# Performance work log

Measured on AMD Instinct MI355X. Metric: run time of the kernel, lower is better.

The kernel has to match this reference:

```python
import jax, jax.numpy as jnp
import numpy as np

B, S, D = 2, 2048, 2048
H, KVH, HD = 16, 4, 128
M = 2  # modalities
THETA = 10000.0
REP = H // KVH


def make_freq_cis(seq_len, head_dim, theta):
    # (S, head_dim//2, 2, 2) rotation matrices [[cos,-sin],[sin,cos]]
    inv = theta ** (-jnp.arange(0, head_dim, 2, dtype=jnp.float32) / head_dim)
    ang = jnp.arange(seq_len, dtype=jnp.float32)[:, None] * inv[None, :]  # (S, hd/2)
    c, s = jnp.cos(ang), jnp.sin(ang)
    row0 = jnp.stack([c, -s], axis=-1)
    row1 = jnp.stack([s, c], axis=-1)
    return jnp.stack([row0, row1], axis=-2)  # (S, hd/2, 2, 2)


def setup_inputs() -> dict:
    key = jax.random.key(0)
    ks = jax.random.split(key, 7)
    std = D ** -0.5
    x = jax.random.normal(ks[0], (B, S, D), dtype=jnp.float32)
    freq_cis = make_freq_cis(S, HD, THETA)
    modality_ids = jax.random.randint(ks[1], (B, S), 0, M, dtype=jnp.int32)
    wq = jax.random.normal(ks[2], (M, D, H * HD), dtype=jnp.float32) * std
    wk = jax.random.normal(ks[3], (M, D, KVH * HD), dtype=jnp.float32) * std
    wv = jax.random.normal(ks[4], (M, D, KVH * HD), dtype=jnp.float32) * std
    wo = jax.random.normal(ks[5], (M, H * HD, D), dtype=jnp.float32) * std
    return {"x": x, "freq_cis": freq_cis, "modality_ids": modality_ids,
            "wq": wq, "wk": wk, "wv": wv, "wo": wo}


def apply_rope(t, freq_cis):
    # t: (B, S, h, HD); freq_cis: (S, HD//2, 2, 2)
    b, s, h, hd = t.shape
    t2 = t.reshape(b, s, h, hd // 2, 2)
    out = jnp.einsum('bshdk,sdjk->bshdj', t2, freq_cis)
    return out.reshape(b, s, h, hd)


def reference(x, freq_cis, modality_ids, wq, wk, wv, wo):
    bsz, seq, dim = x.shape
    onehot = jax.nn.one_hot(modality_ids, M, dtype=x.dtype)  # (B,S,M)
    # per-modality QKV projection, then combine (masks partition tokens)
    q = jnp.einsum('bsm,bsd,mdo->bso', onehot, x, wq).reshape(bsz, seq, H, HD)
    k = jnp.einsum('bsm,bsd,mdo->bso', onehot, x, wk).reshape(bsz, seq, KVH, HD)
    v = jnp.einsum('bsm,bsd,mdo->bso', onehot, x, wv).reshape(bsz, seq, KVH, HD)
    q = apply_rope(q, freq_cis)
    k = apply_rope(k, freq_cis)
    # GQA: repeat_interleave kv heads along head dim
    k = jnp.repeat(k, REP, axis=2)
    v = jnp.repeat(v, REP, axis=2)
    scale = 1.0 / jnp.sqrt(jnp.asarray(HD, dtype=x.dtype))
    scores = jnp.einsum('bqhd,bkhd->bhqk', q, k) * scale
    causal = jnp.tril(jnp.ones((seq, seq), dtype=bool))
    scores = jnp.where(causal[None, None], scores, jnp.finfo(x.dtype).min)
    probs = jax.nn.softmax(scores, axis=-1)
    attn = jnp.einsum('bhqk,bkhd->bqhd', probs, v).reshape(bsz, seq, H * HD)
    # per-modality output projection
    out = jnp.einsum('bsm,bso,moe->bse', onehot, attn, wo)
    return out
```

## Files before the change

### kernel.cpp

```cpp
#include <hip/hip_runtime.h>
#include <stdint.h>

typedef unsigned short u16;
typedef __bf16  bf16x8 __attribute__((ext_vector_type(8), may_alias));
typedef u16     u16x8  __attribute__((ext_vector_type(8), may_alias));
typedef float   f32x4  __attribute__((ext_vector_type(4)));
typedef float   f32x4u __attribute__((ext_vector_type(4), may_alias));

#define Bv   2
#define Sv   2048
#define Dv   2048
#define Hv   16
#define KVHv 4
#define HDv  128
#define Tv   (Bv*Sv)
#define QKVN 3072
#define MAXROWS 4352

__device__ __forceinline__ float b2f(u16 u) {
    union { float f; uint32_t i; } x; x.i = ((uint32_t)u) << 16; return x.f;
}
__device__ __forceinline__ u16 f2b(float f) {
    union { float f; uint32_t u; } x; x.f = f;
    uint32_t r = x.u + 0x7fff + ((x.u >> 16) & 1);
    return (u16)(r >> 16);
}
__device__ __forceinline__ void gload_lds16(const void* g, void* l) {
    __builtin_amdgcn_global_load_lds((__attribute__((address_space(1))) void*)(uintptr_t)g,
                                     (__attribute__((address_space(3))) void*)(uintptr_t)l,
                                     16, 0, 0);
}

__global__ __launch_bounds__(1024) void scan_mod(const int* __restrict__ mod, int* __restrict__ fwd,
                                                 int* __restrict__ inv, int* __restrict__ hdr) {
    __shared__ int cnt[1024];
    const int tid = threadIdx.x;
    int m[4]; int c = 0;
#pragma unroll
    for (int e = 0; e < 4; ++e) { m[e] = mod[tid * 4 + e]; c += (m[e] == 0); }
    cnt[tid] = c;
    __syncthreads();
    for (int off = 1; off < 1024; off <<= 1) {
        int v = (tid >= off) ? cnt[tid - off] : 0;
        __syncthreads();
        cnt[tid] += v;
        __syncthreads();
    }
    const int c0 = cnt[1023];
    const int c0pad = (c0 + 255) & ~255;
    const int c1 = Tv - c0;
    const int total = c0pad + ((c1 + 255) & ~255);
    for (int p = tid; p < MAXROWS; p += 1024) inv[p] = -1;
    __syncthreads();
    const int ex0 = cnt[tid] - c;
    int z = 0;
#pragma unroll
    for (int e = 0; e < 4; ++e) {
        int t = tid * 4 + e;
        int pos;
        if (m[e] == 0) { pos = ex0 + z; ++z; }
        else           { pos = c0pad + (t - (ex0 + z)); }
        fwd[t] = pos;
        inv[pos] = t;
    }
    if (tid == 0) { hdr[0] = total >> 8; hdr[1] = c0pad; hdr[2] = total; }
}

__global__ void gather_cast(const float* __restrict__ x, const int* __restrict__ inv,
                            u16* __restrict__ Xg) {
    int v = blockIdx.x * 256 + threadIdx.x;
    int pos = v >> 8, c8 = (v & 255) * 8;
    int t = inv[pos];
    u16x8 val = {0, 0, 0, 0, 0, 0, 0, 0};
    if (t >= 0) {
        f32x4u a = *(const f32x4u*)&x[(size_t)t * Dv + c8];
        f32x4u b = *(const f32x4u*)&x[(size_t)t * Dv + c8 + 4];
#pragma unroll
        for (int j = 0; j < 4; ++j) { val[j] = f2b(a[j]); val[4 + j] = f2b(b[j]); }
    }
    *(u16x8*)&Xg[(size_t)pos * Dv + c8] = val;
}

__global__ void transpose_cast(const float* __restrict__ in, u16* __restrict__ out, int C,
                               size_t inZ, size_t outZ) {
    in  += (size_t)blockIdx.z * inZ;
    out += (size_t)blockIdx.z * outZ;
    __shared__ u16 tile[64][72];
    const int tr = blockIdx.y * 64, tc = blockIdx.x * 64;
    const int tid = threadIdx.x;
#pragma unroll
    for (int i = 0; i < 4; ++i) {
        int s = tid + 256 * i;
        int r = s >> 4, c4 = (s & 15) * 4;
        f32x4u v = *(const f32x4u*)&in[(size_t)(tr + r) * C + tc + c4];
#pragma unroll
        for (int j = 0; j < 4; ++j) tile[r][c4 + j] = f2b(v[j]);
    }
    __syncthreads();
#pragma unroll
    for (int i = 0; i < 2; ++i) {
        int s = tid + 256 * i;
        int r = s >> 3, c8 = (s & 7) * 8;
        u16x8 v;
#pragma unroll
        for (int j = 0; j < 8; ++j) v[j] = tile[c8 + j][r];
        *(u16x8*)&out[(size_t)(tc + r) * 2048 + tr + c8] = v;
    }
}

__device__ __forceinline__ void store_c(u16* C, size_t idx, float v) { C[idx] = f2b(v); }
__device__ __forceinline__ void store_c(float* C, size_t idx, float v) { C[idx] = v; }

template <typename OutT>
__global__ __launch_bounds__(512, 2) void gemm256(const u16* __restrict__ A,
                                                  const u16* __restrict__ Bt,
                                                  OutT* __restrict__ C,
                                                  const int* __restrict__ inv,
                                                  const int* __restrict__ hdr,
                                                  int Nfull, int ldC) {
    const int total = hdr[2], c0pad = hdr[1];
    const int bm = blockIdx.y * 256;
    if (bm >= total) return;
    const u16* B = Bt + (size_t)((bm >= c0pad) ? 1 : 0) * Nfull * 2048;
    const int bn = blockIdx.x * 256;
    const int tid = threadIdx.x;
    const int wave = tid >> 6, lane = tid & 63;
    const int l15 = lane & 15, l4 = lane >> 4;
    const int wm = wave >> 2;
    const int wn = wave & 3;
    const int bhh = wn >> 1, brr = (wn & 1) * 64;
    const int rsw = l15 & 7;
    __shared__ u16 ldsA[2][2][128 * 64];
    __shared__ u16 ldsB[2][2][128 * 64];
    const int srow = tid >> 3;
    const int ssw  = (tid & 7) ^ (srow & 7);
    const int wofs = wave * 8 * 64;

    f32x4 acc[8][4] = {};

    auto stA = [&](int sl, int h, int jrb, int kt) {
        gload_lds16(A + (size_t)(bm + h * 128 + jrb * 64 + srow) * 2048 + kt * 64 + ssw * 8,
                    &ldsA[sl][h][jrb * 64 * 64 + wofs]);
    };
    auto stB = [&](int sl, int h, int jrb, int kt) {
        gload_lds16(B + (size_t)(bn + h * 128 + jrb * 64 + srow) * 2048 + kt * 64 + ssw * 8,
                    &ldsB[sl][h][jrb * 64 * 64 + wofs]);
    };

    stB(0, 0, 0, 0); stB(0, 0, 1, 0); stB(0, 1, 0, 0); stB(0, 1, 1, 0);
    stA(0, 0, 0, 0); stA(0, 1, 0, 0); stA(0, 0, 1, 0); stA(0, 1, 1, 0);
    asm volatile("s_waitcnt vmcnt(2)" ::: "memory");
    __builtin_amdgcn_s_barrier();
    __builtin_amdgcn_sched_barrier(0);

    for (int kt = 0; kt < 32; ++kt) {
        const int s = kt & 1;
        const bool st = (kt < 31);
        bf16x8 bfr[4][2];
#pragma unroll
        for (int fj = 0; fj < 4; ++fj)
#pragma unroll
            for (int kc = 0; kc < 2; ++kc)
                bfr[fj][kc] = *(const bf16x8*)&ldsB[s][bhh][(brr + fj * 16 + l15) * 64 + ((kc * 4 + l4) ^ rsw) * 8];
#pragma unroll
        for (int q = 0; q < 4; ++q) {
            bf16x8 af[2][2];
#pragma unroll
            for (int fi = 0; fi < 2; ++fi)
#pragma unroll
                for (int kc = 0; kc < 2; ++kc)
                    af[fi][kc] = *(const bf16x8*)&ldsA[s][wm][(q * 32 + fi * 16 + l15) * 64 + ((kc * 4 + l4) ^ rsw) * 8];
            if (st) {
                if      (q == 0) { stB(s ^ 1, 0, 0, kt + 1); stB(s ^ 1, 0, 1, kt + 1); }
                else if (q == 1) { stB(s ^ 1, 1, 0, kt + 1); stB(s ^ 1, 1, 1, kt + 1); }
                else if (q == 2) { stA(s ^ 1, 0, 0, kt + 1); stA(s ^ 1, 1, 0, kt + 1); }
                else             { stA(s ^ 1, 0, 1, kt + 1); stA(s ^ 1, 1, 1, kt + 1); }
            }
            __builtin_amdgcn_s_setprio(1);
#pragma unroll
            for (int kc = 0; kc < 2; ++kc)
#pragma unroll
                for (int fi = 0; fi < 2; ++fi)
#pragma unroll
                    for (int fj = 0; fj < 4; ++fj)
                        acc[q * 2 + fi][fj] = __builtin_amdgcn_mfma_f32_16x16x32_bf16(
                            af[fi][kc], bfr[fj][kc], acc[q * 2 + fi][fj], 0, 0, 0);
            __builtin_amdgcn_s_setprio(0);
            if (q == 1) {
                if (st) asm volatile("s_waitcnt vmcnt(4)" ::: "memory");
                else    asm volatile("s_waitcnt vmcnt(0)" ::: "memory");
                __builtin_amdgcn_sched_barrier(0);
            }
            if (q == 3 && st) {
                asm volatile("s_waitcnt vmcnt(2)" ::: "memory");
                __builtin_amdgcn_sched_barrier(0);
            }
            __builtin_amdgcn_s_barrier();
            __builtin_amdgcn_sched_barrier(0);
        }
    }
#pragma unroll
    for (int fi = 0; fi < 8; ++fi)
#pragma unroll
        for (int r = 0; r < 4; ++r) {
            int row = bm + wm * 128 + fi * 16 + l4 * 4 + r;
            int t = inv[row];
            if (t >= 0) {
#pragma unroll
                for (int fj = 0; fj < 4; ++fj) {
                    int col = bn + wn * 64 + fj * 16 + l15;
                    store_c(C, (size_t)t * ldC + col, acc[fi][fj][r]);
                }
            }
        }
}

__global__ void rope_kernel(u16* __restrict__ QKV, const float* __restrict__ fc) {
    int p = blockIdx.x * 256 + threadIdx.x;
    const int t = p / 1280;
    const int r = p - t * 1280;
    const int s = t & (Sv - 1);
    int col, d2; float scale;
    if (r < 1024) { col = 2 * r;                d2 = r & 63;  scale = 0.12751742f; }
    else          { int rr = r - 1024; col = 2048 + 2 * rr; d2 = rr & 63; scale = 1.0f; }
    u16* ptr = QKV + (size_t)t * QKVN + col;
    float t0 = b2f(ptr[0]), t1 = b2f(ptr[1]);
    f32x4u f = *(const f32x4u*)&fc[((size_t)s * 64 + d2) * 4];
    ptr[0] = f2b((t0 * f[0] + t1 * f[1]) * scale);
    ptr[1] = f2b((t0 * f[2] + t1 * f[3]) * scale);
}

__global__ __launch_bounds__(512) void attn_fwd(const u16* __restrict__ QKV, u16* __restrict__ Ag,
                                                const int* __restrict__ fwd) {
    const int p = blockIdx.x;
    const int h = blockIdx.y, b = blockIdx.z;
    const int kvh = h >> 2;
    const int tid = threadIdx.x, wave = tid >> 6, lane = tid & 63;
    const int wgrp = wave >> 2, wl = wave & 3;
    const int l15 = lane & 15, l4 = lane >> 4;
    const int myqb = wgrp ? (31 - p) : p;
    __shared__ u16 smem[32768];

    bf16x8 qf[4];
    {
        const size_t qrow = (size_t)(b * Sv + myqb * 64 + wl * 16 + l15);
#pragma unroll
        for (int kc = 0; kc < 4; ++kc)
            qf[kc] = *(const bf16x8*)&QKV[qrow * QKVN + h * 128 + kc * 32 + l4 * 8];
    }
    f32x4 oacc[8] = {};
    float mrow = -1e30f;
    float lrow = 0.f;

    const size_t kvbase = (size_t)b * Sv * QKVN + 2048 + kvh * 128;

    {
#pragma unroll
        for (int i = 0; i < 2; ++i) {
            int s_u = wave * 64 + 512 * i;
            int s = s_u + lane;
            int r = s >> 4;
            int kvsrc = (r & 32) | ((r & 12) << 1) | ((r & 16) >> 2) | (r & 3);
            int cs = (s & 15) ^ (r & 7);
            gload_lds16(QKV + kvbase + (size_t)kvsrc * QKVN + cs * 8, &smem[(size_t)s_u * 8]);
        }
        u16x8 vr0 = *(const u16x8*)&QKV[kvbase + 512 + (size_t)lane * QKVN + (0 * 8 + wave) * 8];
        u16x8 vr1 = *(const u16x8*)&QKV[kvbase + 512 + (size_t)lane * QKVN + (1 * 8 + wave) * 8];
#pragma unroll
        for (int jj = 0; jj < 8; ++jj) {
            int d0 = wave * 8 + jj, d1 = (8 + wave) * 8 + jj;
            smem[16384 + d0 * 64 + ((((lane >> 3) ^ jj) << 3) | (lane & 7))] = vr0[jj];
            smem[16384 + d1 * 64 + ((((lane >> 3) ^ jj) << 3) | (lane & 7))] = vr1[jj];
        }
    }
    __syncthreads();

    for (int j = 0; j < 32; ++j) {
        const int cur = j & 1;
        const bool stage_next = (j < 31);
        u16* Kcur = smem + cur * 8192;
        u16* Knxt = smem + (cur ^ 1) * 8192;
        u16* Vcur = smem + 16384 + cur * 8192;
        u16* Vnxt = smem + 16384 + (cur ^ 1) * 8192;
        u16x8 vn0, vn1;
        if (stage_next) {
            const size_t nb = kvbase + (size_t)(j + 1) * 64 * QKVN;
#pragma unroll
            for (int i = 0; i < 2; ++i) {
                int s_u = wave * 64 + 512 * i;
                int s = s_u + lane;
                int r = s >> 4;
                int kvsrc = (r & 32) | ((r & 12) << 1) | ((r & 16) >> 2) | (r & 3);
                int cs = (s & 15) ^ (r & 7);
                gload_lds16(QKV + nb + (size_t)kvsrc * QKVN + cs * 8, &Knxt[(size_t)s_u * 8]);
            }
            vn0 = *(const u16x8*)&QKV[nb + 512 + (size_t)lane * QKVN + (0 * 8 + wave) * 8];
            vn1 = *(const u16x8*)&QKV[nb + 512 + (size_t)lane * QKVN + (1 * 8 + wave) * 8];
        }
        if (j <= myqb) {
            f32x4 sacc[4] = {};
#pragma unroll
            for (int kc = 0; kc < 4; ++kc)
#pragma unroll
                for (int nt = 0; nt < 4; ++nt) {
                    int cs = ((kc * 4 + l4) ^ (l15 & 7));
                    bf16x8 kf = *(const bf16x8*)&Kcur[(nt * 16 + l15) * 128 + cs * 8];
                    sacc[nt] = __builtin_amdgcn_mfma_f32_16x16x32_bf16(kf, qf[kc], sacc[nt], 0, 0, 0);
                }
            if (j == myqb) {
#pragma unroll
                for (int nt = 0; nt < 4; ++nt)
#pragma unroll
                    for (int r = 0; r < 4; ++r)
                        if ((nt >> 1) * 32 + l4 * 8 + (nt & 1) * 4 + r > wl * 16 + l15)
                            sacc[nt][r] = -1e30f;
            }
            f32x4 mv = sacc[0];
#pragma unroll
            for (int nt = 1; nt < 4; ++nt)
#pragma unroll
                for (int r = 0; r < 4; ++r) mv[r] = fmaxf(mv[r], sacc[nt][r]);
            float mx = fmaxf(fmaxf(mv[0], mv[1]), fmaxf(mv[2], mv[3]));
            mx = fmaxf(mx, __shfl_xor(mx, 16, 64));
            mx = fmaxf(mx, __shfl_xor(mx, 32, 64));
            float mnew = fmaxf(mrow, mx);
            float fs = exp2f(mrow - mnew);
            mrow = mnew;
            f32x4 pv = {0.f, 0.f, 0.f, 0.f};
#pragma unroll
            for (int nt = 0; nt < 4; ++nt)
#pragma unroll
                for (int r = 0; r < 4; ++r) {
                    float pe = exp2f(sacc[nt][r] - mnew);
                    sacc[nt][r] = pe;
                    pv[r] += pe;
                }
            float ps = (pv[0] + pv[1]) + (pv[2] + pv[3]);
            ps += __shfl_xor(ps, 16, 64);
            ps += __shfl_xor(ps, 32, 64);
            lrow = lrow * fs + ps;
#pragma unroll
            for (int nt = 0; nt < 8; ++nt)
#pragma unroll
                for (int r = 0; r < 4; ++r) oacc[nt][r] *= fs;
            union { uint32_t w[4]; bf16x8 v; } pb0u, pb1u;
#pragma unroll
            for (int nt = 0; nt < 2; ++nt) {
                asm("v_cvt_pk_bf16_f32 %0, %1, %2" : "=v"(pb0u.w[nt * 2])     : "v"(sacc[nt][0]), "v"(sacc[nt][1]));
                asm("v_cvt_pk_bf16_f32 %0, %1, %2" : "=v"(pb0u.w[nt * 2 + 1]) : "v"(sacc[nt][2]), "v"(sacc[nt][3]));
                asm("v_cvt_pk_bf16_f32 %0, %1, %2" : "=v"(pb1u.w[nt * 2])     : "v"(sacc[nt + 2][0]), "v"(sacc[nt + 2][1]));
                asm("v_cvt_pk_bf16_f32 %0, %1, %2" : "=v"(pb1u.w[nt * 2 + 1]) : "v"(sacc[nt + 2][2]), "v"(sacc[nt + 2][3]));
            }
            bf16x8 pb0 = pb0u.v, pb1 = pb1u.v;
#pragma unroll
            for (int nt = 0; nt < 8; ++nt) {
                int d = nt * 16 + l15;
                bf16x8 v0 = *(const bf16x8*)&Vcur[d * 64 + ((l4 ^ (l15 & 7)) << 3)];
                bf16x8 v1 = *(const bf16x8*)&Vcur[d * 64 + (((4 + l4) ^ (l15 & 7)) << 3)];
                oacc[nt] = __builtin_amdgcn_mfma_f32_16x16x32_bf16(v0, pb0, oacc[nt], 0, 0, 0);
                oacc[nt] = __builtin_amdgcn_mfma_f32_16x16x32_bf16(v1, pb1, oacc[nt], 0, 0, 0);
            }
        }
        if (stage_next) {
#pragma unroll
            for (int jj = 0; jj < 8; ++jj) {
                int d0 = wave * 8 + jj, d1 = (8 + wave) * 8 + jj;
                Vnxt[d0 * 64 + ((((lane >> 3) ^ jj) << 3) | (lane & 7))] = vn0[jj];
                Vnxt[d1 * 64 + ((((lane >> 3) ^ jj) << 3) | (lane & 7))] = vn1[jj];
            }
        }
        __syncthreads();
    }
    {
        u16* epi = smem + wave * (16 * 136);
        float rinv = 1.0f / lrow;
#pragma unroll
        for (int nt = 0; nt < 8; ++nt)
#pragma unroll
            for (int r = 0; r < 4; ++r)
                epi[l15 * 136 + nt * 16 + l4 * 4 + r] = f2b(oacc[nt][r] * rinv);
        const int q = lane >> 2;
        const int rowmap = fwd[b * Sv + myqb * 64 + wl * 16 + q];
#pragma unroll
        for (int it = 0; it < 4; ++it) {
            int dv = (lane & 3) + it * 4;
            u16x8 v = *(const u16x8*)&epi[q * 136 + dv * 8];
            *(u16x8*)&Ag[(size_t)rowmap * 2048 + h * 128 + dv * 8] = v;
        }
    }
}

extern "C" void kernel_launch(void* const* d_in, const int* in_sizes, int n_in,
                              void* d_out, int out_size, void* d_ws, size_t ws_size,
                              hipStream_t stream) {
    const float* x   = (const float*)d_in[0];
    const float* fc  = (const float*)d_in[1];
    const int*   mod = (const int*)d_in[2];
    const float* wq  = (const float*)d_in[3];
    const float* wk  = (const float*)d_in[4];
    const float* wv  = (const float*)d_in[5];
    const float* wo  = (const float*)d_in[6];
    float* out = (float*)d_out;
    char* ws = (char*)d_ws;
    u16* Wqkv_t = (u16*)(ws);
    u16* Wo_t   = (u16*)(ws + 25165824);
    u16* Xg     = (u16*)(ws + 41943040);
    u16* QKV    = (u16*)(ws + 59768832);
    int* fwd    = (int*)(ws + 84934656);
    int* inv    = (int*)(ws + 84951040);
    int* hdr    = (int*)(ws + 84968448);
    u16* Ag     = Xg;

    transpose_cast<<<dim3(32, 32, 2), 256, 0, stream>>>(wq, Wqkv_t, 2048,
        (size_t)2048 * 2048, (size_t)3072 * 2048);
    transpose_cast<<<dim3(8, 32, 2),  256, 0, stream>>>(wk, Wqkv_t + (size_t)2048 * 2048, 512,
        (size_t)2048 * 512,  (size_t)3072 * 2048);
    transpose_cast<<<dim3(8, 32, 2),  256, 0, stream>>>(wv, Wqkv_t + (size_t)2560 * 2048, 512,
        (size_t)2048 * 512,  (size_t)3072 * 2048);
    transpose_cast<<<dim3(32, 32, 2), 256, 0, stream>>>(wo, Wo_t, 2048,
        (size_t)2048 * 2048, (size_t)2048 * 2048);
    scan_mod<<<1, 1024, 0, stream>>>(mod, fwd, inv, hdr);
    gather_cast<<<MAXROWS, 256, 0, stream>>>(x, inv, Xg);
    gemm256<u16><<<dim3(12, 17), 512, 0, stream>>>(Xg, Wqkv_t, QKV, inv, hdr, 3072, 3072);
    rope_kernel<<<20480, 256, 0, stream>>>(QKV, fc);
    attn_fwd<<<dim3(16, 16, 2), 512, 0, stream>>>(QKV, Ag, fwd);
    gemm256<float><<<dim3(8, 17), 512, 0, stream>>>(Ag, Wo_t, out, inv, hdr, 2048, 2048);
}
```

Measured before the change: 230.9 us.

## Vectorize RoPE and give attention blocks contiguous 128-row query tiles

The RoPE kernel now processes 16 bf16 values per thread with 128-bit loads and stores instead of two scalar elements, which cuts the thread count and memory transactions. The attention kernel drops the paired-query-block scheme, where two wave groups took blocks p and 31-p and half the waves idled on masked iterations. Each block now covers one contiguous 128-row query tile and only loops over the KV tiles it needs, so all eight waves share each staged K/V tile. Work per block is now uneven across blocks, and the reversed block index is meant to launch the heavier tiles first.

Result: slower. 263.6 us (+14.2%).

```diff
diff --git a/kernel.cpp b/kernel.cpp
--- a/kernel.cpp
+++ b/kernel.cpp
@@ -216,34 +216,45 @@
 }
 
 __global__ void rope_kernel(u16* __restrict__ QKV, const float* __restrict__ fc) {
-    int p = blockIdx.x * 256 + threadIdx.x;
-    const int t = p / 1280;
-    const int r = p - t * 1280;
+    int p8 = blockIdx.x * 256 + threadIdx.x;
+    const int t = p8 / 160;
+    const int r8 = (p8 - t * 160) * 8;
     const int s = t & (Sv - 1);
-    int col, d2; float scale;
-    if (r < 1024) { col = 2 * r;                d2 = r & 63;  scale = 0.12751742f; }
-    else          { int rr = r - 1024; col = 2048 + 2 * rr; d2 = rr & 63; scale = 1.0f; }
+    int col, d2b; float scale;
+    if (r8 < 1024) { col = 2 * r8;               d2b = r8 & 63;  scale = 0.12751742f; }
+    else           { int rr = r8 - 1024; col = 2048 + 2 * rr; d2b = rr & 63; scale = 1.0f; }
     u16* ptr = QKV + (size_t)t * QKVN + col;
-    float t0 = b2f(ptr[0]), t1 = b2f(ptr[1]);
-    f32x4u f = *(const f32x4u*)&fc[((size_t)s * 64 + d2) * 4];
-    ptr[0] = f2b((t0 * f[0] + t1 * f[1]) * scale);
-    ptr[1] = f2b((t0 * f[2] + t1 * f[3]) * scale);
+    u16x8 va = *(const u16x8*)ptr;
+    u16x8 vb = *(const u16x8*)(ptr + 8);
+    u16 arr[16];
+#pragma unroll
+    for (int i = 0; i < 8; ++i) { arr[i] = va[i]; arr[8 + i] = vb[i]; }
+#pragma unroll
+    for (int i = 0; i < 8; ++i) {
+        float t0 = b2f(arr[2 * i]), t1 = b2f(arr[2 * i + 1]);
+        f32x4u f = *(const f32x4u*)&fc[((size_t)s * 64 + d2b + i) * 4];
+        arr[2 * i]     = f2b((t0 * f[0] + t1 * f[1]) * scale);
+        arr[2 * i + 1] = f2b((t0 * f[2] + t1 * f[3]) * scale);
+    }
+#pragma unroll
+    for (int i = 0; i < 8; ++i) { va[i] = arr[i]; vb[i] = arr[8 + i]; }
+    *(u16x8*)ptr = va;
+    *(u16x8*)(ptr + 8) = vb;
 }
 
 __global__ __launch_bounds__(512) void attn_fwd(const u16* __restrict__ QKV, u16* __restrict__ Ag,
                                                 const int* __restrict__ fwd) {
-    const int p = blockIdx.x;
+    const int qt = 15 - blockIdx.x;
     const int h = blockIdx.y, b = blockIdx.z;
     const int kvh = h >> 2;
     const int tid = threadIdx.x, wave = tid >> 6, lane = tid & 63;
-    const int wgrp = wave >> 2, wl = wave & 3;
     const int l15 = lane & 15, l4 = lane >> 4;
-    const int myqb = wgrp ? (31 - p) : p;
+    const int nj = 2 * qt + 2;
     __shared__ u16 smem[32768];
 
     bf16x8 qf[4];
     {
-        const size_t qrow = (size_t)(b * Sv + myqb * 64 + wl * 16 + l15);
+        const size_t qrow = (size_t)(b * Sv + qt * 128 + wave * 16 + l15);
 #pragma unroll
         for (int kc = 0; kc < 4; ++kc)
             qf[kc] = *(const bf16x8*)&QKV[qrow * QKVN + h * 128 + kc * 32 + l4 * 8];
@@ -275,9 +286,9 @@
     }
     __syncthreads();
 
-    for (int j = 0; j < 32; ++j) {
+    for (int j = 0; j < nj; ++j) {
         const int cur = j & 1;
-        const bool stage_next = (j < 31);
+        const bool stage_next = (j + 1 < nj);
         u16* Kcur = smem + cur * 8192;
         u16* Knxt = smem + (cur ^ 1) * 8192;
         u16* Vcur = smem + 16384 + cur * 8192;
@@ -297,7 +308,7 @@
             vn0 = *(const u16x8*)&QKV[nb + 512 + (size_t)lane * QKVN + (0 * 8 + wave) * 8];
             vn1 = *(const u16x8*)&QKV[nb + 512 + (size_t)lane * QKVN + (1 * 8 + wave) * 8];
         }
-        if (j <= myqb) {
+        {
             f32x4 sacc[4] = {};
 #pragma unroll
             for (int kc = 0; kc < 4; ++kc)
@@ -307,12 +318,13 @@
                     bf16x8 kf = *(const bf16x8*)&Kcur[(nt * 16 + l15) * 128 + cs * 8];
                     sacc[nt] = __builtin_amdgcn_mfma_f32_16x16x32_bf16(kf, qf[kc], sacc[nt], 0, 0, 0);
                 }
-            if (j == myqb) {
+            if (j >= 2 * qt) {
+                const int dq = (j - 2 * qt) * 64 - (wave * 16 + l15);
 #pragma unroll
                 for (int nt = 0; nt < 4; ++nt)
 #pragma unroll
                     for (int r = 0; r < 4; ++r)
-                        if ((nt >> 1) * 32 + l4 * 8 + (nt & 1) * 4 + r > wl * 16 + l15)
+                        if (dq + (nt >> 1) * 32 + l4 * 8 + (nt & 1) * 4 + r > 0)
                             sacc[nt][r] = -1e30f;
             }
             f32x4 mv = sacc[0];
@@ -380,7 +392,7 @@
             for (int r = 0; r < 4; ++r)
                 epi[l15 * 136 + nt * 16 + l4 * 4 + r] = f2b(oacc[nt][r] * rinv);
         const int q = lane >> 2;
-        const int rowmap = fwd[b * Sv + myqb * 64 + wl * 16 + q];
+        const int rowmap = fwd[b * Sv + qt * 128 + wave * 16 + q];
 #pragma unroll
         for (int it = 0; it < 4; ++it) {
             int dv = (lane & 3) + it * 4;
@@ -422,7 +434,7 @@
     scan_mod<<<1, 1024, 0, stream>>>(mod, fwd, inv, hdr);
     gather_cast<<<MAXROWS, 256, 0, stream>>>(x, inv, Xg);
     gemm256<u16><<<dim3(12, 17), 512, 0, stream>>>(Xg, Wqkv_t, QKV, inv, hdr, 3072, 3072);
-    rope_kernel<<<20480, 256, 0, stream>>>(QKV, fc);
+    rope_kernel<<<2560, 256, 0, stream>>>(QKV, fc);
     attn_fwd<<<dim3(16, 16, 2), 512, 0, stream>>>(QKV, Ag, fwd);
     gemm256<float><<<dim3(8, 17), 512, 0, stream>>>(Ag, Wo_t, out, inv, hdr, 2048, 2048);
 }
```
